# Performance work log

Hardware: AMD Instinct MI355X
Metric: run time of the kernel (lower is better)

Reference implementation:

```python
import jax, jax.numpy as jnp
import numpy as np

N_NODES = 100000
NEG_SLOPE = 0.2


def gat_conv(x, W, att_src, att_dst, bias, src, dst, heads, out_ch):
    # x: [N, F_in]; W: [F_in, heads*out_ch]; att_*: [heads, out_ch]; bias: [heads*out_ch]
    N = x.shape[0]
    h = (x @ W).reshape(N, heads, out_ch)                 # [N, H, C]
    a_src = jnp.sum(h * att_src[None], axis=-1)           # [N, H]
    a_dst = jnp.sum(h * att_dst[None], axis=-1)           # [N, H]
    # per-edge unnormalized attention logits (PyG GATConv)
    alpha = jax.nn.leaky_relu(a_src[src] + a_dst[dst], NEG_SLOPE)   # [E, H]
    # scatter-softmax over edges grouped by destination node
    m = jax.ops.segment_max(alpha, dst, num_segments=N)   # [N, H]
    m = jnp.where(jnp.isfinite(m), m, 0.0)
    e = jnp.exp(alpha - m[dst])                           # [E, H]
    s = jax.ops.segment_sum(e, dst, num_segments=N)       # [N, H]
    alpha = e / (s[dst] + 1e-16)
    # weighted scatter-add aggregation of neighbor features
    out = jax.ops.segment_sum(alpha[:, :, None] * h[src], dst, num_segments=N)  # [N, H, C]
    return out.reshape(N, heads * out_ch) + bias


def setup_inputs() -> dict:
    key = jax.random.key(0)
    ks = jax.random.split(key, 10)
    F_in = 128
    x = jax.random.normal(ks[0], (N_NODES, F_in), dtype=jnp.float32)
    edge_index = jax.random.randint(ks[1], (2, 3200000), 0, N_NODES, dtype=jnp.int64)
    g = 0.1
    return {
        "x": x,
        "edge_index": edge_index,
        "W1": jax.random.normal(ks[2], (F_in, 32), jnp.float32) * g,
        "att_src1": jax.random.normal(ks[3], (2, 16), jnp.float32) * g,
        "att_dst1": jax.random.normal(ks[4], (2, 16), jnp.float32) * g,
        "b1": jnp.zeros((32,), jnp.float32),
        "W2": jax.random.normal(ks[5], (32, 2), jnp.float32) * g,
        "att_src2": jax.random.normal(ks[6], (1, 2), jnp.float32) * g,
        "att_dst2": jax.random.normal(ks[7], (1, 2), jnp.float32) * g,
        "b2": jnp.zeros((2,), jnp.float32),
    }


def reference(x, edge_index, W1, att_src1, att_dst1, b1, W2, att_src2, att_dst2, b2):
    N = x.shape[0]
    # add self-loops (PyG GATConv default add_self_loops=True)
    loops = jnp.arange(N, dtype=edge_index.dtype)
    src = jnp.concatenate([edge_index[0], loops])
    dst = jnp.concatenate([edge_index[1], loops])
    h = gat_conv(x, W1, att_src1, att_dst1, b1, src, dst, heads=2, out_ch=16)
    h = jax.nn.elu(h)
    h = gat_conv(h, W2, att_src2, att_dst2, b2, src, dst, heads=1, out_ch=2)
    return jax.nn.log_softmax(h, axis=1)
```

## Files before the change

kernel.cpp:

```cpp
#include <hip/hip_runtime.h>
#include <hip/hip_bf16.h>
#include <hip/hip_fp16.h>

#define LEAK   0.2f
#define NPB    200
#define CAP    8192
#define CAPSH  13
#define SBITS  17
#define SMASK  0x1FFFF
#define CHUNKB 8192

__device__ __forceinline__ unsigned pkh(float a, float b) {
    __half2 h = __floats2half2_rn(a, b);
    return *(unsigned*)&h;
}
__device__ __forceinline__ float2 uph(unsigned u) {
    __half2 h = *(__half2*)&u;
    return __half22float2(h);
}

__global__ __launch_bounds__(512) void kbin(const int* __restrict__ ei, int E, int K,
                                            int* __restrict__ cursor,
                                            int* __restrict__ binned) {
    __shared__ int hist[512], gb[512], lc[512];
    __shared__ int probe;
    int t = threadIdx.x;
    hist[t] = 0;
    if (t == 0) probe = 0;
    __syncthreads();
    if (t < 256) {
        int zc = 0;
#pragma unroll
        for (int j = 0; j < 4; j++) zc += (ei[(t * 4 + j) * 2 + 1] == 0) ? 1 : 0;
        if (zc) atomicAdd(&probe, zc);
    }
    __syncthreads();
    int f = (probe == 1024);
    int e0 = blockIdx.x * CHUNKB;
    int ss[16], dd[16];
#pragma unroll
    for (int i = 0; i < 16; i++) {
        int e = e0 + t + 512 * i;
        ss[i] = -1;
        dd[i] = 0;
        if (e < E) {
            int s, d;
            if (f) { s = ei[2 * e]; d = ei[2 * (e + E)]; }
            else   { s = ei[e];     d = ei[e + E]; }
            ss[i] = s;
            dd[i] = d;
            atomicAdd(&hist[d / NPB], 1);
        }
    }
    __syncthreads();
    int h = hist[t];
    lc[t] = 0;
    if (t < K && h) gb[t] = (t << CAPSH) + atomicAdd(&cursor[t], h);
    __syncthreads();
#pragma unroll
    for (int i = 0; i < 16; i++) {
        if (ss[i] >= 0) {
            int bk = dd[i] / NPB;
            int dloc = dd[i] - bk * NPB;
            int pos = atomicAdd(&lc[bk], 1);
            int gpos = gb[bk] + pos;
            if (gpos < ((bk + 1) << CAPSH))
                binned[gpos] = ss[i] | (dloc << SBITS);
        }
    }
}

__global__ __launch_bounds__(256) void k1(const float* __restrict__ x,
                                          const float* __restrict__ W1,
                                          const float* __restrict__ atts,
                                          const float* __restrict__ attd,
                                          uint2* __restrict__ h1h,
                                          float* __restrict__ a1s,
                                          float* __restrict__ a1d, int N) {
    __shared__ float Ws[128 * 32];
    __shared__ float xs[64 * 132];
    int t = threadIdx.x;
    const float4* W4 = (const float4*)W1;
    float4* Ws4 = (float4*)Ws;
#pragma unroll
    for (int i = 0; i < 4; i++) Ws4[t + 256 * i] = W4[t + 256 * i];
    long long node0 = (long long)blockIdx.x * 64;
    const float4* x4 = (const float4*)x;
    float4* xs4 = (float4*)xs;
#pragma unroll
    for (int i = 0; i < 8; i++) {
        int idx = t + 256 * i;
        int row = idx >> 5, col = idx & 31;
        long long n = node0 + row;
        float4 v = make_float4(0.f, 0.f, 0.f, 0.f);
        if (n < N) v = x4[n * 32 + col];
        xs4[row * 33 + col] = v;
    }
    __syncthreads();

    int cg = t & 7, ns = t >> 3;
    const float4* xr0 = (const float4*)(xs + (ns * 2) * 132);
    const float4* xr1 = (const float4*)(xs + (ns * 2 + 1) * 132);
    float acc0[4] = {0.f, 0.f, 0.f, 0.f}, acc1[4] = {0.f, 0.f, 0.f, 0.f};
#pragma unroll 8
    for (int k4 = 0; k4 < 32; k4++) {
        float4 xa = xr0[k4], xb = xr1[k4];
        float av[4] = {xa.x, xa.y, xa.z, xa.w};
        float bv[4] = {xb.x, xb.y, xb.z, xb.w};
#pragma unroll
        for (int i = 0; i < 4; i++) {
            float4 w = Ws4[(k4 * 4 + i) * 8 + cg];
            acc0[0] = fmaf(av[i], w.x, acc0[0]);
            acc0[1] = fmaf(av[i], w.y, acc0[1]);
            acc0[2] = fmaf(av[i], w.z, acc0[2]);
            acc0[3] = fmaf(av[i], w.w, acc0[3]);
            acc1[0] = fmaf(bv[i], w.x, acc1[0]);
            acc1[1] = fmaf(bv[i], w.y, acc1[1]);
            acc1[2] = fmaf(bv[i], w.z, acc1[2]);
            acc1[3] = fmaf(bv[i], w.w, acc1[3]);
        }
    }
    long long gn0 = node0 + ns * 2, gn1 = gn0 + 1;
    if (gn0 < N) h1h[gn0 * 8 + cg] = make_uint2(pkh(acc0[0], acc0[1]),
                                                pkh(acc0[2], acc0[3]));
    if (gn1 < N) h1h[gn1 * 8 + cg] = make_uint2(pkh(acc1[0], acc1[1]),
                                                pkh(acc1[2], acc1[3]));

    float ps0 = 0.f, pd0 = 0.f, ps1 = 0.f, pd1 = 0.f;
#pragma unroll
    for (int i = 0; i < 4; i++) {
        float aa = atts[cg * 4 + i], dd = attd[cg * 4 + i];
        ps0 = fmaf(acc0[i], aa, ps0);
        pd0 = fmaf(acc0[i], dd, pd0);
        ps1 = fmaf(acc1[i], aa, ps1);
        pd1 = fmaf(acc1[i], dd, pd1);
    }
#pragma unroll
    for (int m = 1; m < 4; m <<= 1) {
        ps0 += __shfl_xor(ps0, m, 64);
        pd0 += __shfl_xor(pd0, m, 64);
        ps1 += __shfl_xor(ps1, m, 64);
        pd1 += __shfl_xor(pd1, m, 64);
    }
    if ((cg & 3) == 0) {
        int hd = cg >> 2;
        if (gn0 < N) { a1s[gn0 * 2 + hd] = ps0; a1d[gn0 * 2 + hd] = pd0; }
        if (gn1 < N) { a1s[gn1 * 2 + hd] = ps1; a1d[gn1 * 2 + hd] = pd1; }
    }
}

__global__ __launch_bounds__(1024) void kfused(const int* __restrict__ cursor,
                                               const int* __restrict__ binned,
                                               const uint2* __restrict__ h1h,
                                               const float* __restrict__ a1s,
                                               const float* __restrict__ a1d,
                                               const float* __restrict__ b1,
                                               const float* __restrict__ W2,
                                               const float* __restrict__ as2,
                                               const float* __restrict__ ad2,
                                               float4* __restrict__ pk,
                                               int* __restrict__ srcs,
                                               int* __restrict__ od, int N) {
    __shared__ int lsrc[CAP];
    __shared__ int ldeg[NPB], lcur[NPB], loff[NPB];
    __shared__ int swt[4];
    int b = blockIdx.x, t = threadIdx.x;
    int node0 = b * NPB;
    int nn = min(NPB, N - node0);
    int cnt = cursor[b];
    if (cnt > CAP) cnt = CAP;
    const int* bb = binned + ((long long)b << CAPSH);
    if (t < NPB) ldeg[t] = 0;
    __syncthreads();
    int pv[8];
#pragma unroll
    for (int j = 0; j < 8; j++) {
        int i = t + 1024 * j;
        pv[j] = (i < cnt) ? bb[i] : -1;
        if (pv[j] >= 0) atomicAdd(&ldeg[pv[j] >> SBITS], 1);
    }
    __syncthreads();
    {
        int v = 0, xsc = 0;
        if (t < 256) {
            v = (t < nn) ? ldeg[t] : 0;
            xsc = v;
#pragma unroll
            for (int o = 1; o < 64; o <<= 1) {
                int y = __shfl_up(xsc, o, 64);
                if ((t & 63) >= o) xsc += y;
            }
            if ((t & 63) == 63) swt[t >> 6] = xsc;
        }
        __syncthreads();
        if (t < 256) {
            int add = 0;
#pragma unroll
            for (int j = 0; j < 4; j++)
                if (j < (t >> 6)) add += swt[j];
            xsc += add;
            if (t < nn) {
                int rel = xsc - v;
                loff[t] = rel;
                lcur[t] = rel;
                od[node0 + t] = rel | (v << 14);
            }
        }
        __syncthreads();
    }
#pragma unroll
    for (int j = 0; j < 8; j++) {
        if (pv[j] >= 0) {
            int pos = atomicAdd(&lcur[pv[j] >> SBITS], 1);
            lsrc[pos] = pv[j] & SMASK;
        }
    }
    __syncthreads();
    for (int i = t; i < cnt; i += 1024) srcs[((long long)b << CAPSH) + i] = lsrc[i];

    int wv = t >> 6, lane = t & 63;
    int e8 = lane >> 3, c4 = lane & 7, hd = c4 >> 2;
    bool wlane = (c4 & 3) == 0;
    for (int ni = wv; ni < nn; ni += 16) {
        int n = node0 + ni;
        float a1dn = a1d[2 * n + hd];
        int base = loff[ni], g = ldeg[ni];
        float4 acc = make_float4(0.f, 0.f, 0.f, 0.f);
        float wsum = 0.f;
        for (int tt = e8 - 1; tt < g; tt += 8) {
            int s = (tt < 0) ? n : lsrc[base + tt];
            float al = a1s[2 * s + hd] + a1dn;
            al = al > 0.f ? al : LEAK * al;
            float w = __expf(al);
            uint2 hb = h1h[(size_t)s * 8 + c4];
            float2 f01 = uph(hb.x), f23 = uph(hb.y);
            acc.x = fmaf(w, f01.x, acc.x);
            acc.y = fmaf(w, f01.y, acc.y);
            acc.z = fmaf(w, f23.x, acc.z);
            acc.w = fmaf(w, f23.y, acc.w);
            if (wlane) wsum += w;
        }
#pragma unroll
        for (int m = 8; m < 64; m <<= 1) {
            acc.x += __shfl_xor(acc.x, m, 64);
            acc.y += __shfl_xor(acc.y, m, 64);
            acc.z += __shfl_xor(acc.z, m, 64);
            acc.w += __shfl_xor(acc.w, m, 64);
            wsum += __shfl_xor(wsum, m, 64);
        }
        float wsH = __shfl(wsum, hd * 4, 64);
        float inv = 1.f / (wsH + 1e-16f);
        float4 bv = ((const float4*)b1)[c4];
        float4 t1;
        t1.x = acc.x * inv + bv.x;
        t1.y = acc.y * inv + bv.y;
        t1.z = acc.z * inv + bv.z;
        t1.w = acc.w * inv + bv.w;
        t1.x = t1.x > 0.f ? t1.x : __expf(t1.x) - 1.f;
        t1.y = t1.y > 0.f ? t1.y : __expf(t1.y) - 1.f;
        t1.z = t1.z > 0.f ? t1.z : __expf(t1.z) - 1.f;
        t1.w = t1.w > 0.f ? t1.w : __expf(t1.w) - 1.f;
        const float4* W24 = (const float4*)W2;
        float4 wA = W24[c4 * 2], wB = W24[c4 * 2 + 1];
        float p0 = t1.x * wA.x + t1.y * wA.z + t1.z * wB.x + t1.w * wB.z;
        float p1 = t1.x * wA.y + t1.y * wA.w + t1.z * wB.y + t1.w * wB.w;
#pragma unroll
        for (int m = 1; m < 8; m <<= 1) {
            p0 += __shfl_xor(p0, m, 64);
            p1 += __shfl_xor(p1, m, 64);
        }
        if (lane == 0)
            pk[n] = make_float4(p0 * as2[0] + p1 * as2[1], p0, p1,
                                p0 * ad2[0] + p1 * ad2[1]);
    }
}

__global__ __launch_bounds__(256) void kagg2(const int* __restrict__ od,
                                             const int* __restrict__ srcs,
                                             const float4* __restrict__ pk,
                                             const float* __restrict__ b2,
                                             float* __restrict__ out, int N) {
    int sub = threadIdx.x >> 5, k = threadIdx.x & 31;
    int n = blockIdx.x * 8 + sub;
    if (n >= N) return;
    float4 pn = pk[n];
    float adn = pn.w;
    int o = od[n];
    int base = ((n / NPB) << CAPSH) + (o & 16383);
    int g = o >> 14;
    float a0 = 0.f, a1v = 0.f, wsm = 0.f;
    for (int e = k - 1; e < g; e += 32) {
        float4 p = (e < 0) ? pn : pk[srcs[base + e]];
        float al = p.x + adn;
        al = al > 0.f ? al : LEAK * al;
        float w = __expf(al);
        a0 = fmaf(w, p.y, a0);
        a1v = fmaf(w, p.z, a1v);
        wsm += w;
    }
#pragma unroll
    for (int m = 1; m < 32; m <<= 1) {
        a0 += __shfl_xor(a0, m, 32);
        a1v += __shfl_xor(a1v, m, 32);
        wsm += __shfl_xor(wsm, m, 32);
    }
    if (k == 0) {
        float inv = 1.f / (wsm + 1e-16f);
        float o0 = a0 * inv + b2[0];
        float o1 = a1v * inv + b2[1];
        float mx = fmaxf(o0, o1);
        float lse = mx + __logf(__expf(o0 - mx) + __expf(o1 - mx));
        ((float2*)out)[n] = make_float2(o0 - lse, o1 - lse);
    }
}

extern "C" void kernel_launch(void* const* d_in, const int* in_sizes, int n_in,
                              void* d_out, int out_size, void* d_ws, size_t ws_size,
                              hipStream_t stream) {
    const float* x   = (const float*)d_in[0];
    const int*   ei  = (const int*)d_in[1];
    const float* W1  = (const float*)d_in[2];
    const float* as1 = (const float*)d_in[3];
    const float* ad1 = (const float*)d_in[4];
    const float* b1  = (const float*)d_in[5];
    const float* W2  = (const float*)d_in[6];
    const float* as2 = (const float*)d_in[7];
    const float* ad2 = (const float*)d_in[8];
    const float* b2  = (const float*)d_in[9];
    float* out = (float*)d_out;

    int N = out_size / 2;
    int E = in_sizes[1] / 2;
    int K = (N + NPB - 1) / NPB;

    float* wsp   = (float*)d_ws;
    float4* pk   = (float4*)wsp;
    uint2* h1h   = (uint2*)(pk + (size_t)N);
    float* a1s   = (float*)(h1h + (size_t)N * 8);
    float* a1d   = a1s + (size_t)N * 2;
    int* od      = (int*)(a1d + (size_t)N * 2);
    int* srcs    = od + N;
    int* binned  = srcs + (size_t)K * CAP;
    int* cursor  = binned + (size_t)K * CAP;

    int nblkB = (E + CHUNKB - 1) / CHUNKB;

    hipMemsetAsync(cursor, 0, K * sizeof(int), stream);
    kbin<<<nblkB, 512, 0, stream>>>(ei, E, K, cursor, binned);
    k1<<<(N + 63) / 64, 256, 0, stream>>>(x, W1, as1, ad1, h1h, a1s, a1d, N);
    kfused<<<K, 1024, 0, stream>>>(cursor, binned, h1h, a1s, a1d,
                                   b1, W2, as2, ad2, pk, srcs, od, N);
    kagg2<<<(N + 7) / 8, 256, 0, stream>>>(od, srcs, pk, b2, out, N);
}
```

Measured before the change: 236.8 us.

## Merge edge binning and first-layer GEMM into one heterogeneous prep kernel

Combines the edge-binning kernel and the x@W1 projection kernel into a single launch, where the first blocks do binning and the remaining blocks do the GEMM, sharing LDS through a union. The GEMM is also restructured: each thread loads a slice of one node's features directly into registers (no x staging in LDS), computes partial products for all 32 outputs, and reduces across 8 lanes with shuffles. This removes one kernel launch and lets the two independent phases overlap on the device. In exchange it adds many cross-lane shuffles and higher register pressure for the 32 accumulators.

```diff
diff --git a/kernel.cpp b/kernel.cpp
--- a/kernel.cpp
+++ b/kernel.cpp
@@ -19,133 +19,141 @@
     return __half22float2(h);
 }
 
-__global__ __launch_bounds__(512) void kbin(const int* __restrict__ ei, int E, int K,
-                                            int* __restrict__ cursor,
-                                            int* __restrict__ binned) {
-    __shared__ int hist[512], gb[512], lc[512];
-    __shared__ int probe;
+struct SMbin  { int hist[512]; int gb[512]; int lc[512]; int probe; };
+struct SMgemm { float Ws[4096]; };
+union  SMprep { SMbin bin; SMgemm gemm; };
+
+__global__ __launch_bounds__(512) void kprep(const int* __restrict__ ei, int E, int K,
+                                             int* __restrict__ cursor,
+                                             int* __restrict__ binned,
+                                             const float* __restrict__ x,
+                                             const float* __restrict__ W1,
+                                             const float* __restrict__ atts,
+                                             const float* __restrict__ attd,
+                                             uint2* __restrict__ h1h,
+                                             float* __restrict__ a1s,
+                                             float* __restrict__ a1d,
+                                             int N, int nblkB) {
+    __shared__ SMprep sm;
     int t = threadIdx.x;
-    hist[t] = 0;
-    if (t == 0) probe = 0;
-    __syncthreads();
-    if (t < 256) {
-        int zc = 0;
-#pragma unroll
-        for (int j = 0; j < 4; j++) zc += (ei[(t * 4 + j) * 2 + 1] == 0) ? 1 : 0;
-        if (zc) atomicAdd(&probe, zc);
-    }
-    __syncthreads();
-    int f = (probe == 1024);
-    int e0 = blockIdx.x * CHUNKB;
-    int ss[16], dd[16];
-#pragma unroll
-    for (int i = 0; i < 16; i++) {
-        int e = e0 + t + 512 * i;
-        ss[i] = -1;
-        dd[i] = 0;
-        if (e < E) {
-            int s, d;
-            if (f) { s = ei[2 * e]; d = ei[2 * (e + E)]; }
-            else   { s = ei[e];     d = ei[e + E]; }
-            ss[i] = s;
-            dd[i] = d;
-            atomicAdd(&hist[d / NPB], 1);
-        }
-    }
-    __syncthreads();
-    int h = hist[t];
-    lc[t] = 0;
-    if (t < K && h) gb[t] = (t << CAPSH) + atomicAdd(&cursor[t], h);
-    __syncthreads();
-#pragma unroll
-    for (int i = 0; i < 16; i++) {
-        if (ss[i] >= 0) {
-            int bk = dd[i] / NPB;
-            int dloc = dd[i] - bk * NPB;
-            int pos = atomicAdd(&lc[bk], 1);
-            int gpos = gb[bk] + pos;
-            if (gpos < ((bk + 1) << CAPSH))
-                binned[gpos] = ss[i] | (dloc << SBITS);
-        }
-    }
-}
-
-__global__ __launch_bounds__(256) void k1(const float* __restrict__ x,
-                                          const float* __restrict__ W1,
-                                          const float* __restrict__ atts,
-                                          const float* __restrict__ attd,
-                                          uint2* __restrict__ h1h,
-                                          float* __restrict__ a1s,
-                                          float* __restrict__ a1d, int N) {
-    __shared__ float Ws[128 * 32];
-    __shared__ float xs[64 * 132];
-    int t = threadIdx.x;
-    const float4* W4 = (const float4*)W1;
-    float4* Ws4 = (float4*)Ws;
-#pragma unroll
-    for (int i = 0; i < 4; i++) Ws4[t + 256 * i] = W4[t + 256 * i];
-    long long node0 = (long long)blockIdx.x * 64;
-    const float4* x4 = (const float4*)x;
-    float4* xs4 = (float4*)xs;
-#pragma unroll
-    for (int i = 0; i < 8; i++) {
-        int idx = t + 256 * i;
-        int row = idx >> 5, col = idx & 31;
-        long long n = node0 + row;
-        float4 v = make_float4(0.f, 0.f, 0.f, 0.f);
-        if (n < N) v = x4[n * 32 + col];
-        xs4[row * 33 + col] = v;
-    }
-    __syncthreads();
-
-    int cg = t & 7, ns = t >> 3;
-    const float4* xr0 = (const float4*)(xs + (ns * 2) * 132);
-    const float4* xr1 = (const float4*)(xs + (ns * 2 + 1) * 132);
-    float acc0[4] = {0.f, 0.f, 0.f, 0.f}, acc1[4] = {0.f, 0.f, 0.f, 0.f};
-#pragma unroll 8
-    for (int k4 = 0; k4 < 32; k4++) {
-        float4 xa = xr0[k4], xb = xr1[k4];
-        float av[4] = {xa.x, xa.y, xa.z, xa.w};
-        float bv[4] = {xb.x, xb.y, xb.z, xb.w};
-#pragma unroll
-        for (int i = 0; i < 4; i++) {
-            float4 w = Ws4[(k4 * 4 + i) * 8 + cg];
-            acc0[0] = fmaf(av[i], w.x, acc0[0]);
-            acc0[1] = fmaf(av[i], w.y, acc0[1]);
-            acc0[2] = fmaf(av[i], w.z, acc0[2]);
-            acc0[3] = fmaf(av[i], w.w, acc0[3]);
-            acc1[0] = fmaf(bv[i], w.x, acc1[0]);
-            acc1[1] = fmaf(bv[i], w.y, acc1[1]);
-            acc1[2] = fmaf(bv[i], w.z, acc1[2]);
-            acc1[3] = fmaf(bv[i], w.w, acc1[3]);
-        }
-    }
-    long long gn0 = node0 + ns * 2, gn1 = gn0 + 1;
-    if (gn0 < N) h1h[gn0 * 8 + cg] = make_uint2(pkh(acc0[0], acc0[1]),
-                                                pkh(acc0[2], acc0[3]));
-    if (gn1 < N) h1h[gn1 * 8 + cg] = make_uint2(pkh(acc1[0], acc1[1]),
-                                                pkh(acc1[2], acc1[3]));
-
-    float ps0 = 0.f, pd0 = 0.f, ps1 = 0.f, pd1 = 0.f;
-#pragma unroll
-    for (int i = 0; i < 4; i++) {
-        float aa = atts[cg * 4 + i], dd = attd[cg * 4 + i];
-        ps0 = fmaf(acc0[i], aa, ps0);
-        pd0 = fmaf(acc0[i], dd, pd0);
-        ps1 = fmaf(acc1[i], aa, ps1);
-        pd1 = fmaf(acc1[i], dd, pd1);
-    }
-#pragma unroll
-    for (int m = 1; m < 4; m <<= 1) {
-        ps0 += __shfl_xor(ps0, m, 64);
-        pd0 += __shfl_xor(pd0, m, 64);
-        ps1 += __shfl_xor(ps1, m, 64);
-        pd1 += __shfl_xor(pd1, m, 64);
-    }
-    if ((cg & 3) == 0) {
-        int hd = cg >> 2;
-        if (gn0 < N) { a1s[gn0 * 2 + hd] = ps0; a1d[gn0 * 2 + hd] = pd0; }
-        if (gn1 < N) { a1s[gn1 * 2 + hd] = ps1; a1d[gn1 * 2 + hd] = pd1; }
+    if (blockIdx.x < nblkB) {
+        SMbin& B = sm.bin;
+        B.hist[t] = 0;
+        if (t == 0) B.probe = 0;
+        __syncthreads();
+        if (t < 256) {
+            int zc = 0;
+#pragma unroll
+            for (int j = 0; j < 4; j++) zc += (ei[(t * 4 + j) * 2 + 1] == 0) ? 1 : 0;
+            if (zc) atomicAdd(&B.probe, zc);
+        }
+        __syncthreads();
+        int f = (B.probe == 1024);
+        int e0 = blockIdx.x * CHUNKB;
+        int ss[16], dd[16];
+#pragma unroll
+        for (int i = 0; i < 16; i++) {
+            int e = e0 + t + 512 * i;
+            ss[i] = -1;
+            dd[i] = 0;
+            if (e < E) {
+                int s, d;
+                if (f) { s = ei[2 * e]; d = ei[2 * (e + E)]; }
+                else   { s = ei[e];     d = ei[e + E]; }
+                ss[i] = s;
+                dd[i] = d;
+                atomicAdd(&B.hist[d / NPB], 1);
+            }
+        }
+        __syncthreads();
+        int h = B.hist[t];
+        B.lc[t] = 0;
+        if (t < K && h) B.gb[t] = (t << CAPSH) + atomicAdd(&cursor[t], h);
+        __syncthreads();
+#pragma unroll
+        for (int i = 0; i < 16; i++) {
+            if (ss[i] >= 0) {
+                int bk = dd[i] / NPB;
+                int dloc = dd[i] - bk * NPB;
+                int pos = atomicAdd(&B.lc[bk], 1);
+                int gpos = B.gb[bk] + pos;
+                if (gpos < ((bk + 1) << CAPSH))
+                    binned[gpos] = ss[i] | (dloc << SBITS);
+            }
+        }
+    } else {
+        SMgemm& G = sm.gemm;
+        float4* Ws4 = (float4*)G.Ws;
+        const float4* W4 = (const float4*)W1;
+        Ws4[t] = W4[t];
+        Ws4[t + 512] = W4[t + 512];
+        __syncthreads();
+        int cg = t & 7, ns = t >> 3;
+        long long node0 = (long long)(blockIdx.x - nblkB) * 64;
+        long long n = node0 + ns;
+        bool valid = (n < N);
+        const float4* x4 = (const float4*)x;
+        float4 xv[4];
+#pragma unroll
+        for (int q = 0; q < 4; q++)
+            xv[q] = valid ? x4[n * 32 + cg + 8 * q]
+                          : make_float4(0.f, 0.f, 0.f, 0.f);
+        float4 acc[8];
+#pragma unroll
+        for (int c4 = 0; c4 < 8; c4++) acc[c4] = make_float4(0.f, 0.f, 0.f, 0.f);
+#pragma unroll
+        for (int q = 0; q < 4; q++) {
+            float xs_[4] = {xv[q].x, xv[q].y, xv[q].z, xv[q].w};
+#pragma unroll
+            for (int i = 0; i < 4; i++) {
+                int k = (cg + 8 * q) * 4 + i;
+#pragma unroll
+                for (int c4 = 0; c4 < 8; c4++) {
+                    float4 w = Ws4[k * 8 + c4];
+                    acc[c4].x = fmaf(xs_[i], w.x, acc[c4].x);
+                    acc[c4].y = fmaf(xs_[i], w.y, acc[c4].y);
+                    acc[c4].z = fmaf(xs_[i], w.z, acc[c4].z);
+                    acc[c4].w = fmaf(xs_[i], w.w, acc[c4].w);
+                }
+            }
+        }
+#pragma unroll
+        for (int m = 1; m < 8; m <<= 1) {
+#pragma unroll
+            for (int c4 = 0; c4 < 8; c4++) {
+                acc[c4].x += __shfl_xor(acc[c4].x, m, 64);
+                acc[c4].y += __shfl_xor(acc[c4].y, m, 64);
+                acc[c4].z += __shfl_xor(acc[c4].z, m, 64);
+                acc[c4].w += __shfl_xor(acc[c4].w, m, 64);
+            }
+        }
+        float4 a = acc[0];
+        switch (cg) {
+            case 1: a = acc[1]; break;
+            case 2: a = acc[2]; break;
+            case 3: a = acc[3]; break;
+            case 4: a = acc[4]; break;
+            case 5: a = acc[5]; break;
+            case 6: a = acc[6]; break;
+            case 7: a = acc[7]; break;
+            default: break;
+        }
+        if (valid)
+            h1h[n * 8 + cg] = make_uint2(pkh(a.x, a.y), pkh(a.z, a.w));
+        float ps = a.x * atts[cg * 4] + a.y * atts[cg * 4 + 1] +
+                   a.z * atts[cg * 4 + 2] + a.w * atts[cg * 4 + 3];
+        float pd = a.x * attd[cg * 4] + a.y * attd[cg * 4 + 1] +
+                   a.z * attd[cg * 4 + 2] + a.w * attd[cg * 4 + 3];
+#pragma unroll
+        for (int m = 1; m < 4; m <<= 1) {
+            ps += __shfl_xor(ps, m, 64);
+            pd += __shfl_xor(pd, m, 64);
+        }
+        if ((cg & 3) == 0 && valid) {
+            int hd = cg >> 2;
+            a1s[n * 2 + hd] = ps;
+            a1d[n * 2 + hd] = pd;
+        }
     }
 }
 
@@ -344,10 +352,12 @@
     int* cursor  = binned + (size_t)K * CAP;
 
     int nblkB = (E + CHUNKB - 1) / CHUNKB;
+    int nblkG = (N + 63) / 64;
 
     hipMemsetAsync(cursor, 0, K * sizeof(int), stream);
-    kbin<<<nblkB, 512, 0, stream>>>(ei, E, K, cursor, binned);
-    k1<<<(N + 63) / 64, 256, 0, stream>>>(x, W1, as1, ad1, h1h, a1s, a1d, N);
+    kprep<<<nblkB + nblkG, 512, 0, stream>>>(ei, E, K, cursor, binned,
+                                             x, W1, as1, ad1, h1h, a1s, a1d,
+                                             N, nblkB);
     kfused<<<K, 1024, 0, stream>>>(cursor, binned, h1h, a1s, a1d,
                                    b1, W2, as2, ad2, pk, srcs, od, N);
     kagg2<<<(N + 7) / 8, 256, 0, stream>>>(od, srcs, pk, b2, out, N);
```

New measurement: 302.9 us. 27.9% more time.

## Aggregate layer two per bin with shared-memory atomics instead of CSR rewrite

Applied to the files above, without the earlier changes.

kfused no longer writes the sorted per-node source lists and degree/offset array back to global memory. The second-layer aggregation becomes a per-bin kernel that reads the raw binned edge list directly and accumulates the weighted sums into shared-memory float atomics, with the self-loop term seeded first. This removes a global write and re-read of about 3.2M source indices plus the offsets array. In exchange it relies on LDS atomics, which may contend on high-degree nodes and make the float summation order nondeterministic.

```diff
diff --git a/kernel.cpp b/kernel.cpp
--- a/kernel.cpp
+++ b/kernel.cpp
@@ -158,9 +158,7 @@
                                                const float* __restrict__ W2,
                                                const float* __restrict__ as2,
                                                const float* __restrict__ ad2,
-                                               float4* __restrict__ pk,
-                                               int* __restrict__ srcs,
-                                               int* __restrict__ od, int N) {
+                                               float4* __restrict__ pk, int N) {
     __shared__ int lsrc[CAP];
     __shared__ int ldeg[NPB], lcur[NPB], loff[NPB];
     __shared__ int swt[4];
@@ -203,7 +201,6 @@
                 int rel = xsc - v;
                 loff[t] = rel;
                 lcur[t] = rel;
-                od[node0 + t] = rel | (v << 14);
             }
         }
         __syncthreads();
@@ -216,7 +213,6 @@
         }
     }
     __syncthreads();
-    for (int i = t; i < cnt; i += 1024) srcs[((long long)b << CAPSH) + i] = lsrc[i];
 
     int wv = t >> 6, lane = t & 63;
     int e8 = lane >> 3, c4 = lane & 7, hd = c4 >> 2;
@@ -275,42 +271,48 @@
     }
 }
 
-__global__ __launch_bounds__(256) void kagg2(const int* __restrict__ od,
-                                             const int* __restrict__ srcs,
-                                             const float4* __restrict__ pk,
-                                             const float* __restrict__ b2,
-                                             float* __restrict__ out, int N) {
-    int sub = threadIdx.x >> 5, k = threadIdx.x & 31;
-    int n = blockIdx.x * 8 + sub;
-    if (n >= N) return;
-    float4 pn = pk[n];
-    float adn = pn.w;
-    int o = od[n];
-    int base = ((n / NPB) << CAPSH) + (o & 16383);
-    int g = o >> 14;
-    float a0 = 0.f, a1v = 0.f, wsm = 0.f;
-    for (int e = k - 1; e < g; e += 32) {
-        float4 p = (e < 0) ? pn : pk[srcs[base + e]];
-        float al = p.x + adn;
+__global__ __launch_bounds__(1024) void kagg2b(const int* __restrict__ cursor,
+                                               const int* __restrict__ binned,
+                                               const float4* __restrict__ pk,
+                                               const float* __restrict__ b2,
+                                               float* __restrict__ out, int N) {
+    __shared__ float la2d[NPB], lw[NPB], l0[NPB], l1[NPB];
+    int b = blockIdx.x, t = threadIdx.x;
+    int node0 = b * NPB;
+    int nn = min(NPB, N - node0);
+    int cnt = cursor[b];
+    if (cnt > CAP) cnt = CAP;
+    const int* bb = binned + ((long long)b << CAPSH);
+    if (t < nn) {
+        float4 p = pk[node0 + t];
+        la2d[t] = p.w;
+        float al = p.x + p.w;
         al = al > 0.f ? al : LEAK * al;
         float w = __expf(al);
-        a0 = fmaf(w, p.y, a0);
-        a1v = fmaf(w, p.z, a1v);
-        wsm += w;
-    }
-#pragma unroll
-    for (int m = 1; m < 32; m <<= 1) {
-        a0 += __shfl_xor(a0, m, 32);
-        a1v += __shfl_xor(a1v, m, 32);
-        wsm += __shfl_xor(wsm, m, 32);
-    }
-    if (k == 0) {
-        float inv = 1.f / (wsm + 1e-16f);
-        float o0 = a0 * inv + b2[0];
-        float o1 = a1v * inv + b2[1];
+        lw[t] = w;
+        l0[t] = w * p.y;
+        l1[t] = w * p.z;
+    }
+    __syncthreads();
+    for (int i = t; i < cnt; i += 1024) {
+        int p = bb[i];
+        int s = p & SMASK, dl = p >> SBITS;
+        float4 ps = pk[s];
+        float al = ps.x + la2d[dl];
+        al = al > 0.f ? al : LEAK * al;
+        float w = __expf(al);
+        atomicAdd(&l0[dl], w * ps.y);
+        atomicAdd(&l1[dl], w * ps.z);
+        atomicAdd(&lw[dl], w);
+    }
+    __syncthreads();
+    if (t < nn) {
+        float inv = 1.f / (lw[t] + 1e-16f);
+        float o0 = l0[t] * inv + b2[0];
+        float o1 = l1[t] * inv + b2[1];
         float mx = fmaxf(o0, o1);
         float lse = mx + __logf(__expf(o0 - mx) + __expf(o1 - mx));
-        ((float2*)out)[n] = make_float2(o0 - lse, o1 - lse);
+        ((float2*)out)[node0 + t] = make_float2(o0 - lse, o1 - lse);
     }
 }
 
@@ -338,9 +340,7 @@
     uint2* h1h   = (uint2*)(pk + (size_t)N);
     float* a1s   = (float*)(h1h + (size_t)N * 8);
     float* a1d   = a1s + (size_t)N * 2;
-    int* od      = (int*)(a1d + (size_t)N * 2);
-    int* srcs    = od + N;
-    int* binned  = srcs + (size_t)K * CAP;
+    int* binned  = (int*)(a1d + (size_t)N * 2);
     int* cursor  = binned + (size_t)K * CAP;
 
     int nblkB = (E + CHUNKB - 1) / CHUNKB;
@@ -349,6 +349,6 @@
     kbin<<<nblkB, 512, 0, stream>>>(ei, E, K, cursor, binned);
     k1<<<(N + 63) / 64, 256, 0, stream>>>(x, W1, as1, ad1, h1h, a1s, a1d, N);
     kfused<<<K, 1024, 0, stream>>>(cursor, binned, h1h, a1s, a1d,
-                                   b1, W2, as2, ad2, pk, srcs, od, N);
-    kagg2<<<(N + 7) / 8, 256, 0, stream>>>(od, srcs, pk, b2, out, N);
-}
+                                   b1, W2, as2, ad2, pk, N);
+    kagg2b<<<K, 1024, 0, stream>>>(cursor, binned, pk, b2, out, N);
+}
```

Measured after the change: 260.2 us. +9.9%, slower.
